# Kernel optimization log

Measured on AMD Instinct MI355X. Metric: run time of the kernel, lower is better.

Reference implementation:

```python
import jax, jax.numpy as jnp
import numpy as np
from jax import lax

B = 16
A = 3
LEVEL_HW = [(200, 200), (100, 100), (50, 50), (25, 25)]
STRIDES = [4, 8, 16, 32]
SIZES = [32.0, 64.0, 128.0, 256.0]
RATIOS = np.array([0.5, 1.0, 2.0])
IMG_H = IMG_W = 800.0
PRE_NMS = 1000          # pre_nms_top_n (testing), applied per level
POST_NMS = 1000         # post_nms_top_n (testing)
NMS_THRESH = 0.7
SCORE_THRESH = 0.0
MIN_SIZE = 1.0
BBOX_XFORM_CLIP = float(np.log(1000.0 / 16.0))  # torchvision BoxCoder clamp
N_PER_LEVEL = [h * w * A for h, w in LEVEL_HW]


def _make_anchors():
    # torchvision-style grid anchors, per-location order matches (H, W, A) flatten
    out = []
    for (h, w), stride, size in zip(LEVEL_HW, STRIDES, SIZES):
        hr = np.sqrt(RATIOS)
        wr = 1.0 / hr
        ws = size * wr
        hs = size * hr
        base = np.stack([-ws / 2, -hs / 2, ws / 2, hs / 2], axis=1)  # [A,4]
        sx = np.arange(w) * stride
        sy = np.arange(h) * stride
        yy, xx = np.meshgrid(sy, sx, indexing="ij")
        shifts = np.stack([xx, yy, xx, yy], axis=-1).reshape(-1, 1, 4)
        out.append((shifts + base[None]).reshape(-1, 4))
    return np.concatenate(out, 0).astype(np.float32)


def setup_inputs():
    key = jax.random.key(0)
    ks = jax.random.split(key, 8)
    inp = {}
    for i, (h, w) in enumerate(LEVEL_HW):
        inp[f"cls{i}"] = jax.random.normal(ks[i], (B, A, h, w), jnp.float32)
        inp[f"reg{i}"] = jax.random.normal(ks[4 + i], (B, A * 4, h, w), jnp.float32)
    inp["anchors"] = jnp.asarray(_make_anchors())
    return inp


def _flat(layer, C):
    # permute_and_flatten: [N, A*C, H, W] -> [N, H*W*A, C]
    n, ac, h, w = layer.shape
    a = ac // C
    return layer.reshape(n, a, C, h, w).transpose(0, 3, 4, 1, 2).reshape(n, h * w * a, C)


def _forward(cls_list, reg_list, anchors):
    obj = jnp.concatenate([_flat(c, 1)[..., 0] for c in cls_list], axis=1)   # [B, K]
    deltas = jnp.concatenate([_flat(r, 4) for r in reg_list], axis=1)        # [B, K, 4]

    # --- BoxCoder.decode, weights (1,1,1,1) ---
    wa = anchors[:, 2] - anchors[:, 0]
    ha = anchors[:, 3] - anchors[:, 1]
    cxa = anchors[:, 0] + 0.5 * wa
    cya = anchors[:, 1] + 0.5 * ha
    dx, dy = deltas[..., 0], deltas[..., 1]
    dw = jnp.minimum(deltas[..., 2], BBOX_XFORM_CLIP)
    dh = jnp.minimum(deltas[..., 3], BBOX_XFORM_CLIP)
    pcx = dx * wa + cxa
    pcy = dy * ha + cya
    pw = jnp.exp(dw) * wa
    ph = jnp.exp(dh) * ha
    props = jnp.stack([pcx - 0.5 * pw, pcy - 0.5 * ph,
                       pcx + 0.5 * pw, pcy + 0.5 * ph], -1)  # [B, K, 4]

    # --- per-level top-k (pre_nms_top_n) ---
    idxs = []
    off = 0
    for n in N_PER_LEVEL:
        k = min(PRE_NMS, n)
        _, ti = lax.top_k(obj[:, off:off + n], k)
        idxs.append(ti + off)
        off += n
    top_idx = jnp.concatenate(idxs, axis=1)  # [B, Nc]
    lvl_full = jnp.concatenate([jnp.full((n,), i, jnp.int32)
                                for i, n in enumerate(N_PER_LEVEL)])
    scores = jax.nn.sigmoid(jnp.take_along_axis(obj, top_idx, axis=1))
    boxes = jnp.take_along_axis(props, top_idx[..., None], axis=1)
    lvl = lvl_full[top_idx]

    # --- clip to image, remove small boxes / score threshold (as validity mask) ---
    x1 = jnp.clip(boxes[..., 0], 0.0, IMG_W)
    y1 = jnp.clip(boxes[..., 1], 0.0, IMG_H)
    x2 = jnp.clip(boxes[..., 2], 0.0, IMG_W)
    y2 = jnp.clip(boxes[..., 3], 0.0, IMG_H)
    boxes = jnp.stack([x1, y1, x2, y2], -1)
    valid = (x2 - x1 >= MIN_SIZE) & (y2 - y1 >= MIN_SIZE) & (scores >= SCORE_THRESH)

    # --- sort by score desc (invalid ranked last) ---
    key = jnp.where(valid, scores, -1.0)
    order = jnp.argsort(-key, axis=1)
    boxes = jnp.take_along_axis(boxes, order[..., None], axis=1)
    scores = jnp.take_along_axis(scores, order, axis=1)
    lvl = jnp.take_along_axis(lvl, order, axis=1)
    valid = jnp.take_along_axis(valid, order, axis=1)

    # --- batched_nms: offset boxes by level so cross-level IoU = 0 ---
    off_mult = max(IMG_H, IMG_W) + 1.0
    boff = boxes + lvl[..., None].astype(boxes.dtype) * off_mult
    areas = (boff[..., 2] - boff[..., 0]) * (boff[..., 3] - boff[..., 1])  # [B, Nc]
    Nc = boff.shape[1]
    pos = jnp.arange(Nc)

    def step(supp, i):
        bi = boff[:, i]                                   # [B, 4]
        keep_i = valid[:, i] & (~supp[:, i])              # [B]
        ix1 = jnp.maximum(boff[..., 0], bi[:, None, 0])
        iy1 = jnp.maximum(boff[..., 1], bi[:, None, 1])
        ix2 = jnp.minimum(boff[..., 2], bi[:, None, 2])
        iy2 = jnp.minimum(boff[..., 3], bi[:, None, 3])
        inter = jnp.maximum(ix2 - ix1, 0.0) * jnp.maximum(iy2 - iy1, 0.0)
        union = areas + areas[:, i][:, None] - inter
        iou = inter / jnp.where(union > 0, union, 1.0)
        sup = keep_i[:, None] & (iou > NMS_THRESH) & (pos > i)[None, :]
        return supp | sup, keep_i

    _, keeps = lax.scan(step, jnp.zeros((boxes.shape[0], Nc), bool), pos)
    keep = keeps.T  # [B, Nc]

    # --- compact kept boxes (already score-sorted) into fixed [B, POST_NMS, ...] ---
    def sel(b, s, k):
        rank = jnp.cumsum(k) - 1
        idx = jnp.where(k & (rank < POST_NMS), rank, POST_NMS)  # overflow -> slot POST
        ob = jnp.zeros((POST_NMS + 1, 4), b.dtype).at[idx].set(b)[:POST_NMS]
        osc = jnp.zeros((POST_NMS + 1,), s.dtype).at[idx].set(s)[:POST_NMS]
        return ob, osc

    return jax.vmap(sel)(boxes, scores, keep)


def reference(cls0, cls1, cls2, cls3, reg0, reg1, reg2, reg3, anchors):
    return _forward([cls0, cls1, cls2, cls3], [reg0, reg1, reg2, reg3], anchors)
```

## Files before the change

kernel.cpp:

```cpp
#include <hip/hip_runtime.h>
#include <cstdint>
#include <cstddef>

typedef uint32_t u32;
typedef uint64_t u64;

#define NB 16
#define POSTN 1000
#define PREN 1000
#define LSEG 1024
#define LCH 16
#define SIDECAP 4096
#define BSIDE 2048
#define TRIPCAP (LSEG * LCH)
#define NPAIR 160
#define NBUCK 8192
#define BSHIFT 19

__constant__ int c_N[4]    = {120000, 30000, 7500, 1875};
__constant__ int c_OFF[4]  = {0, 120000, 150000, 157500};
__constant__ int c_HW[4]   = {40000, 10000, 2500, 625};
__constant__ int c_W[4]    = {200, 100, 50, 25};
__constant__ int c_BASE[4] = {0, 1024, 2048, 3072};

__device__ __forceinline__ u32 ord_bits(float f) {
  u32 u = __float_as_uint(f);
  return (u & 0x80000000u) ? ~u : (u | 0x80000000u);
}
__device__ __forceinline__ float inv_ord(u32 o) {
  u32 bits = (o & 0x80000000u) ? (o ^ 0x80000000u) : ~o;
  return __uint_as_float(bits);
}
__device__ __forceinline__ u64 readlane_u64(u64 v, int l) {
  u32 lo = (u32)__builtin_amdgcn_readlane((int)(u32)v, l);
  u32 hi = (u32)__builtin_amdgcn_readlane((int)(u32)(v >> 32), l);
  return (((u64)hi) << 32) | (u64)lo;
}

__device__ __forceinline__ void slice_map(int bid, int& lvl, int& b, int& e0,
                                          int& nsl) {
  if (bid < 128)      { lvl = 0; b = bid >> 3; e0 = (bid & 7) * 15000; nsl = 15000; }
  else if (bid < 160) { lvl = 1; int t = bid - 128; b = t >> 1; e0 = (t & 1) * 15000; nsl = 15000; }
  else if (bid < 176) { lvl = 2; b = bid - 160; e0 = 0; nsl = 7500; }
  else                { lvl = 3; b = bid - 176; e0 = 0; nsl = 1875; }
}

struct DecBox { float x1, y1, x2, y2; int lvl; bool valid; };

__device__ DecBox decode_box(u32 gid, int b,
    const float* __restrict__ reg0, const float* __restrict__ reg1,
    const float* __restrict__ reg2, const float* __restrict__ reg3,
    const float* __restrict__ anchors) {
  int lvl = (gid < 120000u) ? 0 : (gid < 150000u) ? 1 : (gid < 157500u) ? 2 : 3;
  int local = (int)gid - c_OFF[lvl];
  int a = local % 3;
  int cell = local / 3;
  int w = c_W[lvl];
  int hw = c_HW[lvl];
  int y = cell / w;
  int x = cell - y * w;
  const float* reg = (lvl == 0) ? reg0 : (lvl == 1) ? reg1 : (lvl == 2) ? reg2 : reg3;
  size_t base = ((size_t)(b * 12 + a * 4) * (size_t)w + (size_t)y) * (size_t)w + (size_t)x;
  const float CLIPV = 4.135166556742356f;
  float dx = reg[base];
  float dy = reg[base + (size_t)hw];
  float dwv = fminf(reg[base + 2 * (size_t)hw], CLIPV);
  float dhv = fminf(reg[base + 3 * (size_t)hw], CLIPV);
  float a0 = anchors[(size_t)gid * 4 + 0];
  float a1 = anchors[(size_t)gid * 4 + 1];
  float a2 = anchors[(size_t)gid * 4 + 2];
  float a3 = anchors[(size_t)gid * 4 + 3];
  float wa = __fsub_rn(a2, a0);
  float ha = __fsub_rn(a3, a1);
  float cxa = __fadd_rn(a0, __fmul_rn(0.5f, wa));
  float cya = __fadd_rn(a1, __fmul_rn(0.5f, ha));
  float pcx = __fadd_rn(__fmul_rn(dx, wa), cxa);
  float pcy = __fadd_rn(__fmul_rn(dy, ha), cya);
  float pw = __fmul_rn(expf(dwv), wa);
  float ph = __fmul_rn(expf(dhv), ha);
  float x1 = __fsub_rn(pcx, __fmul_rn(0.5f, pw));
  float y1 = __fsub_rn(pcy, __fmul_rn(0.5f, ph));
  float x2 = __fadd_rn(pcx, __fmul_rn(0.5f, pw));
  float y2 = __fadd_rn(pcy, __fmul_rn(0.5f, ph));
  x1 = fminf(fmaxf(x1, 0.0f), 800.0f);
  y1 = fminf(fmaxf(y1, 0.0f), 800.0f);
  x2 = fminf(fmaxf(x2, 0.0f), 800.0f);
  y2 = fminf(fmaxf(y2, 0.0f), 800.0f);
  DecBox r;
  r.x1 = x1; r.y1 = y1; r.x2 = x2; r.y2 = y2; r.lvl = lvl;
  r.valid = (__fsub_rn(x2, x1) >= 1.0f) && (__fsub_rn(y2, y1) >= 1.0f);
  return r;
}

__global__ void k_zero(float* __restrict__ out, u32* __restrict__ counters,
                       u32* __restrict__ sidecnt, u32* __restrict__ tripcnt,
                       u64* __restrict__ cand_key, u32* __restrict__ rnzl,
                       u32* __restrict__ hist1, u32* __restrict__ state_known,
                       u32* __restrict__ state_kneed) {
  int i = blockIdx.x * blockDim.x + threadIdx.x;
  if (i < NB * POSTN * 5) out[i] = 0.0f;
  if (i < NB * 4096) cand_key[i] = 0ull;
  if (i < 64 * LSEG) rnzl[i] = 0u;
  if (i < 64 * NBUCK) hist1[i] = 0u;
  if (i < 64 * 16) { counters[i] = 0u; sidecnt[i] = 0u; tripcnt[i] = 0u; }
  if (i < 64) { state_known[i] = 0u; state_kneed[i] = (u32)PREN; }
}

__global__ __launch_bounds__(1024) void k_hist1(
    const float* __restrict__ cls0, const float* __restrict__ cls1,
    const float* __restrict__ cls2, const float* __restrict__ cls3,
    u32* __restrict__ hist1) {
  int lvl, b, e0, nsl;
  slice_map(blockIdx.x, lvl, b, e0, nsl);
  const float* cls = (lvl == 0) ? cls0 : (lvl == 1) ? cls1 : (lvl == 2) ? cls2 : cls3;
  const float* cp = cls + (size_t)b * c_N[lvl];
  int tid = threadIdx.x;
  __shared__ u32 h[NBUCK];
  for (int t = tid; t < NBUCK; t += 1024) h[t] = 0u;
  __syncthreads();
  if (lvl != 3) {
    const float4* cp4 = (const float4*)(cp + e0);
    int n4 = nsl >> 2;
    for (int t = tid; t < n4; t += 1024) {
      float4 v = cp4[t];
      atomicAdd(&h[ord_bits(v.x) >> BSHIFT], 1u);
      atomicAdd(&h[ord_bits(v.y) >> BSHIFT], 1u);
      atomicAdd(&h[ord_bits(v.z) >> BSHIFT], 1u);
      atomicAdd(&h[ord_bits(v.w) >> BSHIFT], 1u);
    }
  } else {
    for (int e = e0 + tid; e < e0 + nsl; e += 1024)
      atomicAdd(&h[ord_bits(cp[e]) >> BSHIFT], 1u);
  }
  __syncthreads();
  int task = lvl * 16 + b;
  for (int t = tid; t < NBUCK; t += 1024) {
    u32 v = h[t];
    if (v) atomicAdd(&hist1[task * NBUCK + t], v);
  }
}

__global__ __launch_bounds__(1024) void k_pick1(
    const u32* __restrict__ hist1, u32* __restrict__ state_known,
    u32* __restrict__ state_kneed) {
  int task = blockIdx.x;
  int tid = threadIdx.x;
  __shared__ u32 A[NBUCK], Bb[NBUCK];
  __shared__ int sh_t;
  __shared__ u32 sh_above;
  u32 kneed = (u32)PREN;
  for (int t = tid; t < NBUCK; t += 1024) A[t] = hist1[task * NBUCK + t];
  __syncthreads();
  u32* cur = A;
  u32* nxt = Bb;
  for (int off2 = 1; off2 < NBUCK; off2 <<= 1) {
    for (int t = tid; t < NBUCK; t += 1024)
      nxt[t] = cur[t] + ((t + off2 < NBUCK) ? cur[t + off2] : 0u);
    __syncthreads();
    u32* tmp = cur; cur = nxt; nxt = tmp;
  }
  for (int t = tid; t < NBUCK; t += 1024) {
    u32 s = cur[t];
    u32 above = (t + 1 < NBUCK) ? cur[t + 1] : 0u;
    if (s >= kneed && above < kneed) { sh_t = t; sh_above = above; }
  }
  __syncthreads();
  if (tid == 0) {
    state_known[task] = (u32)sh_t << BSHIFT;
    state_kneed[task] = kneed - sh_above;
  }
}

__global__ __launch_bounds__(1024) void k_collect(
    const float* __restrict__ cls0, const float* __restrict__ cls1,
    const float* __restrict__ cls2, const float* __restrict__ cls3,
    const u32* __restrict__ state_known,
    const float* __restrict__ reg0, const float* __restrict__ reg1,
    const float* __restrict__ reg2, const float* __restrict__ reg3,
    const float* __restrict__ anchors, u32* __restrict__ counters,
    u32* __restrict__ sidecnt, u64* __restrict__ sidebuf,
    u64* __restrict__ cand_key) {
  int lvl, b, e0, nsl;
  slice_map(blockIdx.x, lvl, b, e0, nsl);
  int task = lvl * 16 + b;
  u32 tb = state_known[task] >> BSHIFT;
  const float* cls = (lvl == 0) ? cls0 : (lvl == 1) ? cls1 : (lvl == 2) ? cls2 : cls3;
  const float* cp = cls + (size_t)b * c_N[lvl];
  int tid = threadIdx.x;
  __shared__ u32 ldef[1024];
  __shared__ u32 lside[BSIDE];
  __shared__ u32 cdef, cside, bdef, bside;
  if (tid == 0) { cdef = 0u; cside = 0u; }
  __syncthreads();
  if (lvl != 3) {
    const float4* cp4 = (const float4*)(cp + e0);
    int n4 = nsl >> 2;
    for (int t = tid; t < n4; t += 1024) {
      float4 v4 = cp4[t];
      int ebase = e0 + (t << 2);
#pragma unroll
      for (int c = 0; c < 4; ++c) {
        float f = (c == 0) ? v4.x : (c == 1) ? v4.y : (c == 2) ? v4.z : v4.w;
        u32 bk = ord_bits(f) >> BSHIFT;
        if (bk < tb) continue;
        if (bk > tb) {
          u32 i = atomicAdd(&cdef, 1u);
          if (i < 1024u) ldef[i] = (u32)(ebase + c);
        } else {
          u32 i = atomicAdd(&cside, 1u);
          if (i < (u32)BSIDE) lside[i] = (u32)(ebase + c);
        }
      }
    }
  } else {
    for (int e = e0 + tid; e < e0 + nsl; e += 1024) {
      u32 bk = ord_bits(cp[e]) >> BSHIFT;
      if (bk < tb) continue;
      if (bk > tb) {
        u32 i = atomicAdd(&cdef, 1u);
        if (i < 1024u) ldef[i] = (u32)e;
      } else {
        u32 i = atomicAdd(&cside, 1u);
        if (i < (u32)BSIDE) lside[i] = (u32)e;
      }
    }
  }
  __syncthreads();
  if (tid == 0) bdef = atomicAdd(&counters[task * 16], min(cdef, 1024u));
  if (tid == 1) bside = atomicAdd(&sidecnt[task * 16], min(cside, (u32)BSIDE));
  __syncthreads();
  int hw = c_HW[lvl], off = c_OFF[lvl];
  u32 nd = min(cdef, 1024u);
  for (u32 i = tid; i < nd; i += 1024) {
    int e = (int)ldef[i];
    int a = e / hw;
    int cell = e - a * hw;
    u32 gid = (u32)(off + cell * 3 + a);
    u64 key = ((u64)ord_bits(cp[e]) << 32) | (u32)(~gid);
    DecBox bx = decode_box(gid, b, reg0, reg1, reg2, reg3, anchors);
    u64 skey = bx.valid ? key : (key & 0xFFFFFFFFull);
    u32 slot = bdef + i;
    if (slot < (u32)PREN)
      cand_key[(size_t)b * 4096 + c_BASE[lvl] + slot] = skey;
  }
  u32 ns = min(cside, (u32)BSIDE);
  for (u32 i = tid; i < ns; i += 1024) {
    int e = (int)lside[i];
    int a = e / hw;
    int cell = e - a * hw;
    u32 gid = (u32)(off + cell * 3 + a);
    u64 key = ((u64)ord_bits(cp[e]) << 32) | (u32)(~gid);
    u32 slot = bside + i;
    if (slot < (u32)SIDECAP) sidebuf[(size_t)task * SIDECAP + slot] = key;
  }
}

__global__ __launch_bounds__(1024) void k_finalize(
    const u64* __restrict__ sidebuf, const u32* __restrict__ sidecnt,
    const u32* __restrict__ counters, const u32* __restrict__ state_kneed,
    const float* __restrict__ reg0, const float* __restrict__ reg1,
    const float* __restrict__ reg2, const float* __restrict__ reg3,
    const float* __restrict__ anchors, u64* __restrict__ cand_key) {
  int task = blockIdx.x;
  int lvl = task >> 4;
  int b = task & 15;
  int tid = threadIdx.x;
  u32 nside = min(sidecnt[task * 16], (u32)SIDECAP);
  u32 kneed = state_kneed[task];
  u32 nab = counters[task * 16];
  u32 np2 = 64;
  while (np2 < nside) np2 <<= 1;
  __shared__ u64 sk[SIDECAP];
  for (u32 i = tid; i < np2; i += 1024)
    sk[i] = (i < nside) ? sidebuf[(size_t)task * SIDECAP + i] : 0ull;
  __syncthreads();
  for (u32 k = 2; k <= np2; k <<= 1) {
    for (u32 j = k >> 1; j > 0; j >>= 1) {
      for (u32 t = tid; t < np2 / 2; t += 1024) {
        u32 i = 2u * t - (t & (j - 1u));
        u32 l2 = i | j;
        u64 av = sk[i], bv = sk[l2];
        bool up = ((i & k) == 0u);
        if (up ? (av < bv) : (av > bv)) { sk[i] = bv; sk[l2] = av; }
      }
      __syncthreads();
    }
  }
  if (tid < (int)kneed) {
    u64 key = sk[tid];
    u32 gid = ~((u32)key);
    DecBox bx = decode_box(gid, b, reg0, reg1, reg2, reg3, anchors);
    u64 skey = bx.valid ? key : (key & 0xFFFFFFFFull);
    u32 slot = nab + (u32)tid;
    if (slot < (u32)PREN)
      cand_key[(size_t)b * 4096 + c_BASE[lvl] + slot] = skey;
  }
}

__global__ __launch_bounds__(1024) void k_sortdec(
    u64* __restrict__ cand_key,
    const float* __restrict__ reg0, const float* __restrict__ reg1,
    const float* __restrict__ reg2, const float* __restrict__ reg3,
    const float* __restrict__ anchors,
    float4* __restrict__ sbox, float4* __restrict__ boffA,
    float* __restrict__ area, float* __restrict__ score,
    u64* __restrict__ vmaskl) {
  int bl = blockIdx.x;
  int b = bl >> 2;
  int tid = threadIdx.x;
  __shared__ u64 sk[LSEG];
  sk[tid] = cand_key[(size_t)bl * LSEG + tid];
  __syncthreads();
  for (u32 k = 2; k <= LSEG; k <<= 1) {
    for (u32 j = k >> 1; j > 0; j >>= 1) {
      if (tid < LSEG / 2) {
        u32 t = (u32)tid;
        u32 i = 2u * t - (t & (j - 1u));
        u32 l2 = i | j;
        u64 av = sk[i], bv = sk[l2];
        bool up = ((i & k) == 0u);
        if (up ? (av < bv) : (av > bv)) { sk[i] = bv; sk[l2] = av; }
      }
      __syncthreads();
    }
  }
  u64 key = sk[tid];
  cand_key[(size_t)bl * LSEG + tid] = key;
  float4 bx4 = make_float4(0.f, 0.f, 0.f, 0.f);
  float4 bo4 = make_float4(0.f, 0.f, 0.f, 0.f);
  float ar = 0.f, sc = 0.f;
  bool vflag = false;
  if (key != 0ull) {
    u32 gid = ~((u32)key);
    vflag = (key >> 32) != 0ull;
    DecBox bx = decode_box(gid, b, reg0, reg1, reg2, reg3, anchors);
    bx4 = make_float4(bx.x1, bx.y1, bx.x2, bx.y2);
    float offv = __fmul_rn((float)bx.lvl, 801.0f);
    bo4 = make_float4(__fadd_rn(bx.x1, offv), __fadd_rn(bx.y1, offv),
                      __fadd_rn(bx.x2, offv), __fadd_rn(bx.y2, offv));
    ar = __fmul_rn(__fsub_rn(bo4.z, bo4.x), __fsub_rn(bo4.w, bo4.y));
    if (vflag) {
      float logit = inv_ord((u32)(key >> 32));
      sc = 1.0f / (1.0f + expf(-logit));
    }
  }
  size_t gi = (size_t)bl * LSEG + tid;
  sbox[gi] = bx4;
  boffA[gi] = bo4;
  area[gi] = ar;
  score[gi] = sc;
  u64 bal = __ballot(vflag ? 1 : 0);
  if ((tid & 63) == 0) vmaskl[bl * LCH + (tid >> 6)] = bal;
}

#define RPB 16
__global__ __launch_bounds__(256) void k_maskl(
    const float4* __restrict__ boffA, const float* __restrict__ area,
    ulonglong2* __restrict__ trip, u32* __restrict__ tripcnt,
    u32* __restrict__ rnzl) {
  const double Bd = 0x1.6666661p-1;
  int bg = blockIdx.x;
  int bl = bg / NPAIR;
  int p = bg - bl * NPAIR;
  int chunk, g;
  if (p < 16)      { chunk = 0; g = p; }
  else if (p < 48) { chunk = 1; g = p - 16; }
  else if (p < 96) { chunk = 2; g = p - 48; }
  else             { chunk = 3; g = p - 96; }
  int row0 = g * RPB;
  int tid = threadIdx.x;
  int wave = tid >> 6;
  int lane = tid & 63;
  __shared__ float4 rb[RPB];
  __shared__ float ra[RPB];
  __shared__ ulonglong2 stage[RPB * 4];
  __shared__ u32 scount, sbase;
  if (tid == 0) scount = 0u;
  if (tid < RPB) {
    rb[tid] = boffA[(size_t)bl * LSEG + row0 + tid];
    ra[tid] = area[(size_t)bl * LSEG + row0 + tid];
  }
  __syncthreads();
  int wword = chunk * 4 + wave;
  int wmaxj = chunk * 256 + wave * 64 + 63;
  int j = chunk * 256 + tid;
  float4 cb = boffA[(size_t)bl * LSEG + j];
  float ca = area[(size_t)bl * LSEG + j];
  if (wmaxj > row0) {
#pragma unroll
    for (int rr = 0; rr < RPB; ++rr) {
      int i = row0 + rr;
      if (wmaxj <= i) continue;
      float4 rbb = rb[rr];
      float ria = ra[rr];
      float ix1 = fmaxf(cb.x, rbb.x);
      float iy1 = fmaxf(cb.y, rbb.y);
      float ix2 = fminf(cb.z, rbb.z);
      float iy2 = fminf(cb.w, rbb.w);
      float inter = __fmul_rn(fmaxf(__fsub_rn(ix2, ix1), 0.0f),
                              fmaxf(__fsub_rn(iy2, iy1), 0.0f));
      float uni = __fsub_rn(__fadd_rn(ca, ria), inter);
      bool pred = (j > i) && (inter > 0.0f) &&
                  ((double)inter >= Bd * (double)uni);
      u64 bal = __ballot(pred ? 1 : 0);
      if (lane == 0 && bal) {
        u32 sidx = atomicAdd(&scount, 1u);
        ulonglong2 e;
        e.x = bal;
        e.y = (u64)(u32)(i * LCH + wword);
        stage[sidx] = e;
        atomicOr(&rnzl[(size_t)bl * LSEG + i], 1u << wword);
      }
    }
  }
  __syncthreads();
  if (tid == 0 && scount) sbase = atomicAdd(&tripcnt[bl * 16], scount);
  __syncthreads();
  for (u32 t = tid; t < scount; t += 256)
    trip[(size_t)bl * TRIPCAP + sbase + t] = stage[t];
}

__global__ __launch_bounds__(64) void k_nmsl(
    const ulonglong2* __restrict__ trip, const u32* __restrict__ tripcnt,
    const u32* __restrict__ rnzl, const u64* __restrict__ vmaskl,
    const u64* __restrict__ cand_key,
    u64* __restrict__ keptkeys, u32* __restrict__ keptpos,
    u32* __restrict__ keptcnt) {
  int bl = blockIdx.x;
  int lane = threadIdx.x;
  extern __shared__ char smem[];
  u64* lmask = (u64*)smem;
  u32* rnzL  = (u32*)(smem + (size_t)LSEG * LCH * 8);
  ulonglong2 z2; z2.x = 0ull; z2.y = 0ull;
  ulonglong2* lm2 = (ulonglong2*)lmask;
  for (int t = lane; t < LSEG * LCH / 2; t += 64) lm2[t] = z2;
  for (int t = lane; t < LSEG; t += 64) rnzL[t] = rnzl[(size_t)bl * LSEG + t];
  u64 vword = (lane < LCH) ? vmaskl[bl * LCH + lane] : 0ull;
  __syncthreads();
  u32 tc = tripcnt[bl * 16];
  for (u32 t = lane; t < tc; t += 64) {
    ulonglong2 e = trip[(size_t)bl * TRIPCAP + t];
    lmask[(u32)e.y] = e.x;
  }
  __syncthreads();
  u64 supp = 0ull;
  u64 keep = 0ull;
  for (int W = 0; W < LCH; ++W) {
    int c0 = W << 6;
    u32 rzW = rnzL[c0 + lane];
    u64 dchW = lmask[(size_t)(c0 + lane) * LCH + W];
    u64 s = __shfl(supp, W);
    u64 v = __shfl(vword, W);
    u64 pending = v & ~s;
    u64 kw = 0ull;
    u64 suppressors = __ballot((dchW & pending) != 0ull) & pending;
    while (pending) {
      u64 sp = pending & suppressors;
      if (!sp) { kw |= pending; break; }
      int q = __builtin_ctzll(sp);
      u64 below = pending & ((1ull << q) - 1ull);
      kw |= below | (1ull << q);
      u64 supq = readlane_u64(dchW, q);
      pending &= ~supq & ~below & ~(1ull << q);
    }
    u64 kk = __ballot(((rzW >> W) >> 1) != 0u) & kw;
    bool ld = (lane < LCH);
    u64 acc = 0ull;
    while (kk) {
      int q0 = __builtin_ctzll(kk); kk &= kk - 1ull;
      u64 m0 = ld ? lmask[(size_t)(c0 + q0) * LCH + lane] : 0ull;
      u64 m1 = 0ull, m2 = 0ull, m3 = 0ull;
      if (kk) {
        int q1 = __builtin_ctzll(kk); kk &= kk - 1ull;
        m1 = ld ? lmask[(size_t)(c0 + q1) * LCH + lane] : 0ull;
      }
      if (kk) {
        int q2 = __builtin_ctzll(kk); kk &= kk - 1ull;
        m2 = ld ? lmask[(size_t)(c0 + q2) * LCH + lane] : 0ull;
      }
      if (kk) {
        int q3 = __builtin_ctzll(kk); kk &= kk - 1ull;
        m3 = ld ? lmask[(size_t)(c0 + q3) * LCH + lane] : 0ull;
      }
      acc |= (m0 | m1) | (m2 | m3);
    }
    supp |= acc;
    if (lane == W) keep = kw;
  }
  int pc = __popcll(keep);
  int incl = pc;
  for (int d = 1; d < 64; d <<= 1) {
    int t = __shfl_up(incl, d);
    if (lane >= d) incl += t;
  }
  int r = incl - pc;
  u64 kk = keep;
  while (kk) {
    int bit = __builtin_ctzll(kk);
    kk &= kk - 1ull;
    int p = lane * 64 + bit;
    keptkeys[(size_t)bl * LSEG + r] = cand_key[(size_t)bl * LSEG + p];
    keptpos[(size_t)bl * LSEG + r] = (u32)p;
    ++r;
  }
  if (lane == 63) keptcnt[bl] = (u32)incl;
}

__global__ __launch_bounds__(1024) void k_out(
    const u64* __restrict__ keptkeys, const u32* __restrict__ keptpos,
    const u32* __restrict__ keptcnt, const float4* __restrict__ sbox,
    const float* __restrict__ score, float* __restrict__ out) {
  int bl = blockIdx.x;
  int b = bl >> 2;
  int l = bl & 3;
  int r = threadIdx.x;
  u32 cnt = keptcnt[bl];
  if (r >= (int)cnt) return;
  u64 K = keptkeys[(size_t)bl * LSEG + r];
  int rank = r;
#pragma unroll
  for (int dl = 0; dl < 4; ++dl) {
    if (dl == l) continue;
    int obl = (b << 2) | dl;
    const u64* arr = keptkeys + (size_t)obl * LSEG;
    int lo = 0, hi = (int)keptcnt[obl];
    while (lo < hi) {
      int mid = (lo + hi) >> 1;
      if (arr[mid] > K) lo = mid + 1; else hi = mid;
    }
    rank += lo;
  }
  if (rank < POSTN) {
    u32 p = keptpos[(size_t)bl * LSEG + r];
    float4 bx = sbox[(size_t)bl * LSEG + p];
    size_t ob = ((size_t)b * POSTN + (size_t)rank) * 4;
    out[ob + 0] = bx.x;
    out[ob + 1] = bx.y;
    out[ob + 2] = bx.z;
    out[ob + 3] = bx.w;
    out[(size_t)NB * POSTN * 4 + (size_t)b * POSTN + (size_t)rank] =
        score[(size_t)bl * LSEG + p];
  }
}

extern "C" void kernel_launch(void* const* d_in, const int* in_sizes, int n_in,
                              void* d_out, int out_size, void* d_ws, size_t ws_size,
                              hipStream_t stream) {
  const float* cls0 = (const float*)d_in[0];
  const float* reg0 = (const float*)d_in[1];
  const float* cls1 = (const float*)d_in[2];
  const float* reg1 = (const float*)d_in[3];
  const float* cls2 = (const float*)d_in[4];
  const float* reg2 = (const float*)d_in[5];
  const float* cls3 = (const float*)d_in[6];
  const float* reg3 = (const float*)d_in[7];
  const float* anchors = (const float*)d_in[8];
  float* out = (float*)d_out;

  char* ws = (char*)d_ws;
  size_t off = 0;
  auto take = [&](size_t bytes) -> void* {
    off = (off + 255) & ~(size_t)255;
    void* p = ws + off;
    off += bytes;
    return p;
  };
  ulonglong2* trip = (ulonglong2*)take((size_t)64 * TRIPCAP * 16);
  u64* sidebuf   = (u64*)take((size_t)64 * SIDECAP * 8);
  u32* rnzl      = (u32*)take((size_t)64 * LSEG * 4);
  u64* cand_key  = (u64*)take((size_t)NB * 4096 * 8);
  float4* sbox   = (float4*)take((size_t)64 * LSEG * 16);
  float4* boffA  = (float4*)take((size_t)64 * LSEG * 16);
  float* area    = (float*)take((size_t)64 * LSEG * 4);
  float* score   = (float*)take((size_t)64 * LSEG * 4);
  u64* vmaskl    = (u64*)take((size_t)64 * LCH * 8);
  u64* keptkeys  = (u64*)take((size_t)64 * LSEG * 8);
  u32* keptpos   = (u32*)take((size_t)64 * LSEG * 4);
  u32* keptcnt   = (u32*)take((size_t)64 * 4);
  u32* hist1     = (u32*)take((size_t)64 * NBUCK * 4);
  u32* counters  = (u32*)take((size_t)64 * 16 * 4);
  u32* sidecnt   = (u32*)take((size_t)64 * 16 * 4);
  u32* tripcnt   = (u32*)take((size_t)64 * 16 * 4);
  u32* state_known = (u32*)take((size_t)64 * 4);
  u32* state_kneed = (u32*)take((size_t)64 * 4);
  (void)ws_size; (void)in_sizes; (void)n_in; (void)out_size;

  k_zero<<<2048, 256, 0, stream>>>(out, counters, sidecnt, tripcnt, cand_key,
                                   rnzl, hist1, state_known, state_kneed);
  k_hist1<<<192, 1024, 0, stream>>>(cls0, cls1, cls2, cls3, hist1);
  k_pick1<<<64, 1024, 0, stream>>>(hist1, state_known, state_kneed);
  k_collect<<<192, 1024, 0, stream>>>(cls0, cls1, cls2, cls3, state_known,
                                      reg0, reg1, reg2, reg3, anchors,
                                      counters, sidecnt, sidebuf, cand_key);
  k_finalize<<<64, 1024, 0, stream>>>(sidebuf, sidecnt, counters, state_kneed,
                                      reg0, reg1, reg2, reg3, anchors,
                                      cand_key);
  k_sortdec<<<64, 1024, 0, stream>>>(cand_key, reg0, reg1, reg2, reg3,
                                     anchors, sbox, boffA, area, score,
                                     vmaskl);
  k_maskl<<<64 * NPAIR, 256, 0, stream>>>(boffA, area, trip, tripcnt, rnzl);
  k_nmsl<<<64, 64, 135168, stream>>>(trip, tripcnt, rnzl, vmaskl, cand_key,
                                     keptkeys, keptpos, keptcnt);
  k_out<<<64, 1024, 0, stream>>>(keptkeys, keptpos, keptcnt, sbox, score, out);
}
```

Measured before the change: 131.7 us.

## Fuse side-buffer finalize into sortdec and speed up threshold-pick prefix scan

Merges the per-task side-buffer bitonic sort and decode into the per-segment sort kernel, so candidate keys are assembled in shared memory instead of being written to global memory and reloaded by a separate launch. Zeroing of the rnzl buffer moves into the fused kernel as well. The histogram threshold pick now does per-thread sums of 8 buckets followed by a 1024-entry suffix scan, replacing a 13-pass scan over 8192 entries. The fused kernel uses more shared memory per block.

```diff
diff --git a/kernel.cpp b/kernel.cpp
--- a/kernel.cpp
+++ b/kernel.cpp
@@ -94,13 +94,12 @@
 
 __global__ void k_zero(float* __restrict__ out, u32* __restrict__ counters,
                        u32* __restrict__ sidecnt, u32* __restrict__ tripcnt,
-                       u64* __restrict__ cand_key, u32* __restrict__ rnzl,
+                       u64* __restrict__ cand_key,
                        u32* __restrict__ hist1, u32* __restrict__ state_known,
                        u32* __restrict__ state_kneed) {
   int i = blockIdx.x * blockDim.x + threadIdx.x;
   if (i < NB * POSTN * 5) out[i] = 0.0f;
   if (i < NB * 4096) cand_key[i] = 0ull;
-  if (i < 64 * LSEG) rnzl[i] = 0u;
   if (i < 64 * NBUCK) hist1[i] = 0u;
   if (i < 64 * 16) { counters[i] = 0u; sidecnt[i] = 0u; tripcnt[i] = 0u; }
   if (i < 64) { state_known[i] = 0u; state_kneed[i] = (u32)PREN; }
@@ -145,24 +144,34 @@
     u32* __restrict__ state_kneed) {
   int task = blockIdx.x;
   int tid = threadIdx.x;
-  __shared__ u32 A[NBUCK], Bb[NBUCK];
+  __shared__ u32 h[NBUCK];
+  __shared__ u32 spA[1024];
+  __shared__ u32 spB[1024];
   __shared__ int sh_t;
   __shared__ u32 sh_above;
   u32 kneed = (u32)PREN;
-  for (int t = tid; t < NBUCK; t += 1024) A[t] = hist1[task * NBUCK + t];
-  __syncthreads();
-  u32* cur = A;
-  u32* nxt = Bb;
-  for (int off2 = 1; off2 < NBUCK; off2 <<= 1) {
-    for (int t = tid; t < NBUCK; t += 1024)
-      nxt[t] = cur[t] + ((t + off2 < NBUCK) ? cur[t + off2] : 0u);
+  for (int t = tid; t < NBUCK; t += 1024) h[t] = hist1[task * NBUCK + t];
+  __syncthreads();
+  int base = tid << 3;
+  u32 part = 0;
+#pragma unroll
+  for (int j = 0; j < 8; ++j) part += h[base + j];
+  spA[tid] = part;
+  __syncthreads();
+  u32* cur = spA;
+  u32* nxt = spB;
+  for (int off = 1; off < 1024; off <<= 1) {
+    u32 v = cur[tid] + ((tid + off < 1024) ? cur[tid + off] : 0u);
+    nxt[tid] = v;
     __syncthreads();
     u32* tmp = cur; cur = nxt; nxt = tmp;
   }
-  for (int t = tid; t < NBUCK; t += 1024) {
-    u32 s = cur[t];
-    u32 above = (t + 1 < NBUCK) ? cur[t + 1] : 0u;
-    if (s >= kneed && above < kneed) { sh_t = t; sh_above = above; }
+  u32 suf = (tid + 1 < 1024) ? cur[tid + 1] : 0u;
+#pragma unroll
+  for (int j = 7; j >= 0; --j) {
+    u32 s = suf + h[base + j];
+    if (s >= kneed && suf < kneed) { sh_t = base + j; sh_above = suf; }
+    suf = s;
   }
   __syncthreads();
   if (tid == 0) {
@@ -255,61 +264,56 @@
   }
 }
 
-__global__ __launch_bounds__(1024) void k_finalize(
-    const u64* __restrict__ sidebuf, const u32* __restrict__ sidecnt,
-    const u32* __restrict__ counters, const u32* __restrict__ state_kneed,
+__global__ __launch_bounds__(1024) void k_sortdec(
+    u64* __restrict__ cand_key, const u64* __restrict__ sidebuf,
+    const u32* __restrict__ sidecnt, const u32* __restrict__ counters,
+    const u32* __restrict__ state_kneed,
     const float* __restrict__ reg0, const float* __restrict__ reg1,
     const float* __restrict__ reg2, const float* __restrict__ reg3,
-    const float* __restrict__ anchors, u64* __restrict__ cand_key) {
-  int task = blockIdx.x;
-  int lvl = task >> 4;
-  int b = task & 15;
+    const float* __restrict__ anchors,
+    float4* __restrict__ sbox, float4* __restrict__ boffA,
+    float* __restrict__ area, float* __restrict__ score,
+    u64* __restrict__ vmaskl, u32* __restrict__ rnzl) {
+  int bl = blockIdx.x;
+  int b = bl >> 2;
+  int lvl = bl & 3;
+  int task = lvl * 16 + b;
   int tid = threadIdx.x;
+  rnzl[(size_t)bl * LSEG + tid] = 0u;
+  __shared__ u64 sside[SIDECAP];
+  __shared__ u64 sk[LSEG];
   u32 nside = min(sidecnt[task * 16], (u32)SIDECAP);
   u32 kneed = state_kneed[task];
   u32 nab = counters[task * 16];
   u32 np2 = 64;
   while (np2 < nside) np2 <<= 1;
-  __shared__ u64 sk[SIDECAP];
   for (u32 i = tid; i < np2; i += 1024)
-    sk[i] = (i < nside) ? sidebuf[(size_t)task * SIDECAP + i] : 0ull;
+    sside[i] = (i < nside) ? sidebuf[(size_t)task * SIDECAP + i] : 0ull;
   __syncthreads();
   for (u32 k = 2; k <= np2; k <<= 1) {
     for (u32 j = k >> 1; j > 0; j >>= 1) {
       for (u32 t = tid; t < np2 / 2; t += 1024) {
         u32 i = 2u * t - (t & (j - 1u));
         u32 l2 = i | j;
-        u64 av = sk[i], bv = sk[l2];
+        u64 av = sside[i], bv = sside[l2];
         bool up = ((i & k) == 0u);
-        if (up ? (av < bv) : (av > bv)) { sk[i] = bv; sk[l2] = av; }
+        if (up ? (av < bv) : (av > bv)) { sside[i] = bv; sside[l2] = av; }
       }
       __syncthreads();
     }
   }
   if (tid < (int)kneed) {
-    u64 key = sk[tid];
+    u64 key = sside[tid];
     u32 gid = ~((u32)key);
     DecBox bx = decode_box(gid, b, reg0, reg1, reg2, reg3, anchors);
-    u64 skey = bx.valid ? key : (key & 0xFFFFFFFFull);
-    u32 slot = nab + (u32)tid;
-    if (slot < (u32)PREN)
-      cand_key[(size_t)b * 4096 + c_BASE[lvl] + slot] = skey;
-  }
-}
-
-__global__ __launch_bounds__(1024) void k_sortdec(
-    u64* __restrict__ cand_key,
-    const float* __restrict__ reg0, const float* __restrict__ reg1,
-    const float* __restrict__ reg2, const float* __restrict__ reg3,
-    const float* __restrict__ anchors,
-    float4* __restrict__ sbox, float4* __restrict__ boffA,
-    float* __restrict__ area, float* __restrict__ score,
-    u64* __restrict__ vmaskl) {
-  int bl = blockIdx.x;
-  int b = bl >> 2;
-  int tid = threadIdx.x;
-  __shared__ u64 sk[LSEG];
-  sk[tid] = cand_key[(size_t)bl * LSEG + tid];
+    sside[tid] = bx.valid ? key : (key & 0xFFFFFFFFull);
+  }
+  u64 defk = (tid < (int)nab)
+                 ? cand_key[(size_t)b * 4096 + c_BASE[lvl] + tid] : 0ull;
+  __syncthreads();
+  u64 kv = defk;
+  if (tid >= (int)nab && tid < (int)(nab + kneed)) kv = sside[tid - nab];
+  sk[tid] = kv;
   __syncthreads();
   for (u32 k = 2; k <= LSEG; k <<= 1) {
     for (u32 j = k >> 1; j > 0; j >>= 1) {
@@ -586,18 +590,16 @@
   (void)ws_size; (void)in_sizes; (void)n_in; (void)out_size;
 
   k_zero<<<2048, 256, 0, stream>>>(out, counters, sidecnt, tripcnt, cand_key,
-                                   rnzl, hist1, state_known, state_kneed);
+                                   hist1, state_known, state_kneed);
   k_hist1<<<192, 1024, 0, stream>>>(cls0, cls1, cls2, cls3, hist1);
   k_pick1<<<64, 1024, 0, stream>>>(hist1, state_known, state_kneed);
   k_collect<<<192, 1024, 0, stream>>>(cls0, cls1, cls2, cls3, state_known,
                                       reg0, reg1, reg2, reg3, anchors,
                                       counters, sidecnt, sidebuf, cand_key);
-  k_finalize<<<64, 1024, 0, stream>>>(sidebuf, sidecnt, counters, state_kneed,
-                                      reg0, reg1, reg2, reg3, anchors,
-                                      cand_key);
-  k_sortdec<<<64, 1024, 0, stream>>>(cand_key, reg0, reg1, reg2, reg3,
+  k_sortdec<<<64, 1024, 0, stream>>>(cand_key, sidebuf, sidecnt, counters,
+                                     state_kneed, reg0, reg1, reg2, reg3,
                                      anchors, sbox, boffA, area, score,
-                                     vmaskl);
+                                     vmaskl, rnzl);
   k_maskl<<<64 * NPAIR, 256, 0, stream>>>(boffA, area, trip, tripcnt, rnzl);
   k_nmsl<<<64, 64, 135168, stream>>>(trip, tripcnt, rnzl, vmaskl, cand_key,
                                      keptkeys, keptpos, keptcnt);
```

New measurement: 125.9 us (median of 2 runs). -4.4%, faster.
